# Optimization experiments

Hardware: AMD Instinct MI355X
Metric: run time of the kernel (lower is better)

The kernel has to match this reference:

```python
import jax, jax.numpy as jnp
import numpy as np

S, HID, H, KV, D = 2048, 3584, 16, 8, 256
WINDOW = 1024
SOFTCAP = 50.0
SCALING = 256 ** (-0.5)  # query_pre_attn_scalar ** -0.5
EPS = 1e-6
ROPE_THETA = 10000.0


def _rope_tables(seq_len, dim, theta):
    inv_freq = 1.0 / (theta ** (np.arange(0, dim, 2, dtype=np.float32) / dim))
    t = np.arange(seq_len, dtype=np.float32)
    freqs = np.outer(t, inv_freq)            # [S, D/2]
    emb = np.concatenate([freqs, freqs], -1)  # [S, D]
    return jnp.asarray(np.cos(emb)), jnp.asarray(np.sin(emb))


def setup_inputs() -> dict:
    key = jax.random.key(0)
    ks = jax.random.split(key, 3)
    hidden_states = jax.random.normal(ks[0], (S, HID), jnp.float32)
    w_qkv = jax.random.normal(ks[1], (HID, (H + 2 * KV) * D), jnp.float32) * (HID ** -0.5)
    w_o = jax.random.normal(ks[2], (H * D, HID), jnp.float32) * ((H * D) ** -0.5)
    q_norm_w = jnp.zeros((D,), jnp.float32)  # gemma norm stores weight as (1 + w)
    k_norm_w = jnp.zeros((D,), jnp.float32)
    cos, sin = _rope_tables(S, D, ROPE_THETA)
    return {"hidden_states": hidden_states, "w_qkv": w_qkv, "w_o": w_o,
            "q_norm_w": q_norm_w, "k_norm_w": k_norm_w, "cos": cos, "sin": sin}


def _rms_norm(x, w):
    # gemma-style: fp32 norm, scale by (1 + w); x: [S, h, D]
    xf = x.astype(jnp.float32)
    var = jnp.mean(xf * xf, axis=-1, keepdims=True)
    return (xf * jax.lax.rsqrt(var + EPS) * (1.0 + w)).astype(x.dtype)


def _rotate_half(x):
    x1, x2 = jnp.split(x, 2, axis=-1)
    return jnp.concatenate([-x2, x1], axis=-1)


def _apply_rope(x, cos, sin):
    # x: [S, h, D]; cos/sin: [S, D]
    c = cos[:, None, :]
    s = sin[:, None, :]
    return x * c + _rotate_half(x) * s


def reference(hidden_states, w_qkv, w_o, q_norm_w, k_norm_w, cos, sin):
    qkv = hidden_states @ w_qkv                      # [S, (H+2KV)*D]
    q = qkv[:, : H * D].reshape(S, H, D)
    k = qkv[:, H * D: (H + KV) * D].reshape(S, KV, D)
    v = qkv[:, (H + KV) * D:].reshape(S, KV, D)

    q = _rms_norm(q, q_norm_w)                       # gemma3 q_norm
    k = _rms_norm(k, k_norm_w)                       # gemma3 k_norm
    q = _apply_rope(q, cos, sin)
    k = _apply_rope(k, cos, sin)

    # GQA: expand KV heads to H
    rep = H // KV
    k = jnp.repeat(k, rep, axis=1)                   # [S, H, D]
    v = jnp.repeat(v, rep, axis=1)

    scores = jnp.einsum('shd,thd->hst', q, k) * SCALING  # [H, S, S]
    scores = SOFTCAP * jnp.tanh(scores / SOFTCAP)        # logit softcapping

    i = jnp.arange(S)[:, None]
    j = jnp.arange(S)[None, :]
    allowed = (j <= i) & ((i - j) < WINDOW)              # causal + sliding window
    scores = jnp.where(allowed[None], scores, jnp.float32(-1e30))

    attn = jax.nn.softmax(scores, axis=-1)
    out = jnp.einsum('hst,thd->shd', attn, v).reshape(S, H * D)
    return out @ w_o                                     # [S, HID]
```

## Files before the change

### kernel.cpp

```cpp
#include <hip/hip_runtime.h>
#include <hip/hip_bf16.h>
#include <math.h>

typedef __attribute__((ext_vector_type(8))) short short8;
typedef __attribute__((ext_vector_type(4))) float floatx4;
typedef unsigned short u16;

typedef __attribute__((address_space(1))) const void* gas_ptr;
typedef __attribute__((address_space(3))) void* las_ptr;

__device__ __forceinline__ float bf2f(u16 h) {
  union { unsigned u; float f; } v; v.u = ((unsigned)h) << 16; return v.f;
}
__device__ __forceinline__ u16 f2bf(float f) {
  union { float f; unsigned u; } v; v.f = f;
  unsigned r = v.u + 0x7FFFu + ((v.u >> 16) & 1u);
  return (u16)(r >> 16);
}
__device__ __forceinline__ float ldf_dyn(const void* p, size_t i, bool f32) {
  return f32 ? ((const float*)p)[i] : bf2f(((const u16*)p)[i]);
}
__device__ __forceinline__ short8 load8_dyn(const void* p, size_t idx, bool f32) {
  if (f32) {
    const float* f = (const float*)p;
    float4 a = *(const float4*)(f + idx);
    float4 b = *(const float4*)(f + idx + 4);
    short8 r;
    r[0] = (short)f2bf(a.x); r[1] = (short)f2bf(a.y);
    r[2] = (short)f2bf(a.z); r[3] = (short)f2bf(a.w);
    r[4] = (short)f2bf(b.x); r[5] = (short)f2bf(b.y);
    r[6] = (short)f2bf(b.z); r[7] = (short)f2bf(b.w);
    return r;
  }
  return *(const short8*)((const u16*)p + idx);
}
__device__ __forceinline__ void gl_lds16(const u16* g, u16* l) {
  __builtin_amdgcn_global_load_lds((gas_ptr)g, (las_ptr)l, 16, 0, 0);
}

__global__ void probe_dtype_kernel(const void* hidden, int* flag) {
  __shared__ int cnt;
  if (threadIdx.x == 0) cnt = 0;
  __syncthreads();
  const u16* h = (const u16*)hidden;
  int local = 0;
  for (int i = threadIdx.x; i < 8192; i += 256) {
    u16 u = h[i];
    int e = (u >> 7) & 0xFF;
    if ((e >= 64 && e <= 160) || (u & 0x7FFF) == 0) local++;
  }
  atomicAdd(&cnt, local);
  __syncthreads();
  if (threadIdx.x == 0) *flag = (cnt < 7700) ? 1 : 0;
}

__global__ __launch_bounds__(256) void convert_dyn_kernel(
    const void* __restrict__ src, u16* __restrict__ dst, size_t n,
    const int* __restrict__ flagp)
{
  const bool f32 = (*flagp != 0);
  size_t i = ((size_t)blockIdx.x * 256 + threadIdx.x) * 8;
  if (i < n) *(short8*)(dst + i) = load8_dyn(src, i, f32);
}

__global__ __launch_bounds__(256) void transpose_dyn_kernel(
    const void* __restrict__ src, u16* __restrict__ dst, int R, int C,
    const int* __restrict__ flagp)
{
  const bool f32 = (*flagp != 0);
  const int c0 = blockIdx.x * 64, r0 = blockIdx.y * 64;
  __shared__ __attribute__((aligned(16))) u16 T[64][72];
  const int tid = threadIdx.x;
#pragma unroll
  for (int i = 0; i < 2; i++) {
    int t = tid + i * 256;
    int r = t >> 3, cc = (t & 7) << 3;
    *(short8*)(&T[r][cc]) = load8_dyn(src, (size_t)(r0 + r) * C + c0 + cc, f32);
  }
  __syncthreads();
#pragma unroll
  for (int i = 0; i < 2; i++) {
    int t = tid + i * 256;
    int cr = t >> 3, rc = (t & 7) << 3;
    __attribute__((aligned(16))) u16 tmp[8];
#pragma unroll
    for (int j = 0; j < 8; j++) tmp[j] = T[rc + j][cr];
    *(short8*)(dst + (size_t)(c0 + cr) * R + r0 + rc) = *(const short8*)tmp;
  }
}

#define BAR() __builtin_amdgcn_s_barrier()
#define SCB() __builtin_amdgcn_sched_barrier(0)
#define LGKM0() do { asm volatile("s_waitcnt lgkmcnt(0)" ::: "memory"); SCB(); } while (0)
#define VMW(n) do { asm volatile("s_waitcnt vmcnt(" #n ")" ::: "memory"); SCB(); } while (0)

#define STG_AU(s, u, t) \
  gl_lds16(pa + (size_t)((u) * 64) * K + (size_t)(t) * 64, \
           ldsw + (s) * 32768 + (u) * 4096)
#define STG_BU(s, u, t) \
  gl_lds16(pb + (size_t)((u) * 64) * K + (size_t)(t) * 64, \
           ldsw + (s) * 32768 + 16384 + (u) * 4096)

#define RD_FA(s, miH) do { \
  _Pragma("unroll") \
  for (int m2 = 0; m2 < 4; m2++) { \
    const u16* _r = LDS + (s) * 32768 + wm * 8192 + (miH) * 4096 + m2 * 1024 + lane15 * 64; \
    fa[m2][0] = *(const short8*)(_r + colA0); \
    fa[m2][1] = *(const short8*)(_r + colA1); \
  } \
} while (0)
#define RD_FB(s, niH) do { \
  _Pragma("unroll") \
  for (int n2 = 0; n2 < 2; n2++) { \
    const u16* _r = LDS + (s) * 32768 + 16384 + wn * 4096 + (niH) * 2048 + n2 * 1024 + lane15 * 64; \
    fb[niH][n2][0] = *(const short8*)(_r + colA0); \
    fb[niH][n2][1] = *(const short8*)(_r + colA1); \
  } \
} while (0)
#define MFMA_Q(miH, niH) do { \
  __builtin_amdgcn_s_setprio(1); \
  _Pragma("unroll") \
  for (int m2 = 0; m2 < 4; m2++) \
    _Pragma("unroll") \
    for (int n2 = 0; n2 < 2; n2++) { \
      acc[(miH) * 4 + m2][(niH) * 2 + n2] = __builtin_amdgcn_mfma_f32_16x16x32_bf16( \
          fa[m2][0], fb[niH][n2][0], acc[(miH) * 4 + m2][(niH) * 2 + n2], 0, 0, 0); \
      acc[(miH) * 4 + m2][(niH) * 2 + n2] = __builtin_amdgcn_mfma_f32_16x16x32_bf16( \
          fa[m2][1], fb[niH][n2][1], acc[(miH) * 4 + m2][(niH) * 2 + n2], 0, 0, 0); \
    } \
  __builtin_amdgcn_s_setprio(0); \
  SCB(); \
} while (0)

__global__ __launch_bounds__(512, 2) void gemm8p_kernel(
    const u16* __restrict__ A, const u16* __restrict__ BT, u16* __restrict__ C,
    int M, int N, int K)
{
  __shared__ __attribute__((aligned(16))) u16 LDS[65536];
  const int tid = threadIdx.x;
  const int wave = tid >> 6, lane = tid & 63;
  const int lane15 = lane & 15, quad = lane >> 4;
  const int wm = wave >> 2, wn = wave & 3;
  const int m0 = blockIdx.y * 256, n0 = blockIdx.x * 256;

  const int rloc = wave * 8 + (lane >> 3);
  const int sxor = lane >> 3;
  const int csw = ((lane & 7) ^ sxor) * 8;
  const u16* pa = A + (size_t)(m0 + rloc) * K + csw;
  const u16* pb = BT + (size_t)(n0 + rloc) * K + csw;
  u16* ldsw = LDS + wave * 512;

  const int swz = lane15 & 7;
  const int colA0 = (quad ^ swz) * 8;
  const int colA1 = ((4 + quad) ^ swz) * 8;

  floatx4 acc[8][4];
#pragma unroll
  for (int i = 0; i < 8; i++)
#pragma unroll
    for (int j = 0; j < 4; j++) acc[i][j] = (floatx4){0.f, 0.f, 0.f, 0.f};
  short8 fa[4][2], fb[2][2][2];

  const int NT = K >> 6, NI = NT >> 1;

  STG_AU(0, 0, 0); STG_AU(0, 2, 0);
  STG_BU(0, 0, 0); STG_BU(0, 1, 0);
  STG_BU(0, 2, 0); STG_BU(0, 3, 0);
  STG_AU(0, 1, 0); STG_AU(0, 3, 0);
  STG_AU(1, 0, 1); STG_AU(1, 2, 1);
  STG_BU(1, 0, 1); STG_BU(1, 1, 1);
  STG_BU(1, 2, 1); STG_BU(1, 3, 1);
  VMW(8);
  BAR();

  for (int i = 0; i < NI - 1; i++) {
    const int t1 = 2 * i + 1, t2 = 2 * i + 2, t3 = 2 * i + 3;
    RD_FA(0, 0); RD_FB(0, 0);
    STG_AU(1, 1, t1); STG_AU(1, 3, t1);
    BAR(); LGKM0(); MFMA_Q(0, 0); BAR();
    RD_FB(0, 1);
    STG_AU(0, 0, t2); STG_AU(0, 2, t2);
    BAR(); LGKM0(); MFMA_Q(0, 1); VMW(10); BAR();
    RD_FA(0, 1);
    STG_BU(0, 0, t2); STG_BU(0, 1, t2);
    BAR(); LGKM0(); MFMA_Q(1, 1); BAR();
    STG_BU(0, 2, t2); STG_BU(0, 3, t2);
    BAR(); MFMA_Q(1, 0); VMW(8); BAR();
    RD_FA(1, 0); RD_FB(1, 0);
    STG_AU(0, 1, t2); STG_AU(0, 3, t2);
    BAR(); LGKM0(); MFMA_Q(0, 0); BAR();
    RD_FB(1, 1);
    STG_AU(1, 0, t3); STG_AU(1, 2, t3);
    BAR(); LGKM0(); MFMA_Q(0, 1); VMW(10); BAR();
    RD_FA(1, 1);
    STG_BU(1, 0, t3); STG_BU(1, 1, t3);
    BAR(); LGKM0(); MFMA_Q(1, 1); BAR();
    STG_BU(1, 2, t3); STG_BU(1, 3, t3);
    BAR(); MFMA_Q(1, 0); VMW(8); BAR();
  }

  {
    const int tL = NT - 1;
    RD_FA(0, 0); RD_FB(0, 0);
    STG_AU(1, 1, tL); STG_AU(1, 3, tL);
    BAR(); LGKM0(); MFMA_Q(0, 0); BAR();
    RD_FB(0, 1);
    BAR(); LGKM0(); MFMA_Q(0, 1); VMW(8); BAR();
    RD_FA(0, 1);
    BAR(); LGKM0(); MFMA_Q(1, 1); BAR();
    BAR(); MFMA_Q(1, 0); VMW(2); BAR();
    RD_FA(1, 0); RD_FB(1, 0);
    BAR(); LGKM0(); MFMA_Q(0, 0); BAR();
    RD_FB(1, 1);
    BAR(); LGKM0(); MFMA_Q(0, 1); VMW(0); BAR();
    RD_FA(1, 1);
    BAR(); LGKM0(); MFMA_Q(1, 1); BAR();
    BAR(); MFMA_Q(1, 0);
  }

#pragma unroll
  for (int mi = 0; mi < 8; mi++)
#pragma unroll
    for (int rr = 0; rr < 4; rr++) {
      int m = m0 + wm * 128 + mi * 16 + quad * 4 + rr;
      u16* crow = C + (size_t)m * N + n0 + wn * 64;
#pragma unroll
      for (int ni = 0; ni < 4; ni++) crow[ni * 16 + lane15] = f2bf(acc[mi][ni][rr]);
    }
}

__global__ __launch_bounds__(256) void gemm_bt_kernel(
    const u16* __restrict__ A, const u16* __restrict__ BT, void* __restrict__ C,
    int M, int N, int K, const int* __restrict__ flagp, int cdyn)
{
  __shared__ __attribute__((aligned(16))) u16 As[128 * 32];
  __shared__ __attribute__((aligned(16))) u16 Bs[128 * 32];
  const int tid = threadIdx.x;
  const int wave = tid >> 6, lane = tid & 63;
  const int lane15 = lane & 15, quad = lane >> 4;
  const int wr = (wave >> 1) * 64, wc = (wave & 1) * 64;
  const int m0 = blockIdx.y * 128, n0 = blockIdx.x * 128;

  const int ch0 = wave * 64 + lane;
  const int ch1 = ch0 + 256;
  const int sr0 = ch0 >> 2, sk0 = (ch0 & 3) << 3;
  const int sr1 = ch1 >> 2, sk1 = (ch1 & 3) << 3;
  u16* ldsA0 = &As[wave * 512];
  u16* ldsA1 = &As[2048 + wave * 512];
  u16* ldsB0 = &Bs[wave * 512];
  u16* ldsB1 = &Bs[2048 + wave * 512];
  const u16* pa0 = A + (size_t)(m0 + sr0) * K + sk0;
  const u16* pa1 = A + (size_t)(m0 + sr1) * K + sk1;
  const u16* pb0 = BT + (size_t)(n0 + sr0) * K + sk0;
  const u16* pb1 = BT + (size_t)(n0 + sr1) * K + sk1;

  floatx4 zero = {0.0f, 0.0f, 0.0f, 0.0f};
  floatx4 acc[4][4];
#pragma unroll
  for (int i = 0; i < 4; i++)
#pragma unroll
    for (int j = 0; j < 4; j++) acc[i][j] = zero;

  for (int k0 = 0; k0 < K; k0 += 32) {
    gl_lds16(pa0, ldsA0); gl_lds16(pa1, ldsA1);
    gl_lds16(pb0, ldsB0); gl_lds16(pb1, ldsB1);
    pa0 += 32; pa1 += 32; pb0 += 32; pb1 += 32;
    __syncthreads();
    short8 af[4], bfr[4];
#pragma unroll
    for (int mi = 0; mi < 4; mi++)
      af[mi] = *(const short8*)(&As[(wr + mi * 16 + lane15) * 32 + quad * 8]);
#pragma unroll
    for (int ni = 0; ni < 4; ni++)
      bfr[ni] = *(const short8*)(&Bs[(wc + ni * 16 + lane15) * 32 + quad * 8]);
#pragma unroll
    for (int mi = 0; mi < 4; mi++)
#pragma unroll
      for (int ni = 0; ni < 4; ni++)
        acc[mi][ni] = __builtin_amdgcn_mfma_f32_16x16x32_bf16(
            af[mi], bfr[ni], acc[mi][ni], 0, 0, 0);
    __syncthreads();
  }
  const bool cf32 = cdyn && (*flagp != 0);
  if (cf32) {
    float* Cf = (float*)C;
#pragma unroll
    for (int mi = 0; mi < 4; mi++)
#pragma unroll
      for (int r = 0; r < 4; r++) {
        int m = m0 + wr + mi * 16 + quad * 4 + r;
        float* crow = Cf + (size_t)m * N + n0 + wc;
#pragma unroll
        for (int ni = 0; ni < 4; ni++) crow[ni * 16 + lane15] = acc[mi][ni][r];
      }
  } else {
    u16* Cb = (u16*)C;
#pragma unroll
    for (int mi = 0; mi < 4; mi++)
#pragma unroll
      for (int r = 0; r < 4; r++) {
        int m = m0 + wr + mi * 16 + quad * 4 + r;
        u16* crow = Cb + (size_t)m * N + n0 + wc;
#pragma unroll
        for (int ni = 0; ni < 4; ni++) crow[ni * 16 + lane15] = f2bf(acc[mi][ni][r]);
      }
  }
}

__global__ __launch_bounds__(256) void normrope_kernel(
    u16* __restrict__ qkv, const void* __restrict__ qw,
    const void* __restrict__ kw, const void* __restrict__ cosb,
    const void* __restrict__ sinb, const int* __restrict__ flagp)
{
  const bool f32 = (*flagp != 0);
  const int s = blockIdx.x;
  const int wave = threadIdx.x >> 6, lane = threadIdx.x & 63;
  const int hh = blockIdx.y * 4 + wave;
  const int col = (hh < 16) ? hh * 256 : 4096 + (hh - 16) * 256;
  const void* w = (hh < 16) ? qw : kw;
  u16* row = qkv + (size_t)s * 8192 + col;

  float x[4];
#pragma unroll
  for (int j = 0; j < 4; j++) x[j] = bf2f(row[lane + j * 64]);

  float ss = x[0] * x[0] + x[1] * x[1] + x[2] * x[2] + x[3] * x[3];
#pragma unroll
  for (int off = 32; off > 0; off >>= 1) ss += __shfl_xor(ss, off);
  float inv = rsqrtf(ss * (1.0f / 256.0f) + 1e-6f);

  float y[4];
#pragma unroll
  for (int j = 0; j < 4; j++)
    y[j] = x[j] * inv * (1.0f + ldf_dyn(w, lane + j * 64, f32));
  float rot[4] = {-y[2], -y[3], y[0], y[1]};
#pragma unroll
  for (int j = 0; j < 4; j++) {
    int d = lane + j * 64;
    float c = ldf_dyn(cosb, (size_t)s * 256 + d, f32);
    float sn = ldf_dyn(sinb, (size_t)s * 256 + d, f32);
    row[d] = f2bf(y[j] * c + rot[j] * sn);
  }
}

__global__ __launch_bounds__(256) void vtrans_kernel(
    const u16* __restrict__ qkv, u16* __restrict__ vT)
{
  const int s0 = blockIdx.x * 64, d0 = blockIdx.y * 64, kv = blockIdx.z;
  __shared__ __attribute__((aligned(16))) u16 T[64][72];
  const int tid = threadIdx.x;
#pragma unroll
  for (int i = 0; i < 2; i++) {
    int c = tid + i * 256;
    int r = c >> 3, dc = (c & 7) << 3;
    *(short8*)(&T[r][dc]) =
        *(const short8*)(qkv + (size_t)(s0 + r) * 8192 + 6144 + kv * 256 + d0 + dc);
  }
  __syncthreads();
#pragma unroll
  for (int i = 0; i < 2; i++) {
    int c = tid + i * 256;
    int dr = c >> 3, sc = (c & 7) << 3;
    __attribute__((aligned(16))) u16 tmp[8];
#pragma unroll
    for (int j = 0; j < 8; j++) tmp[j] = T[sc + j][dr];
    *(short8*)(vT + (size_t)kv * 524288 + (size_t)(d0 + dr) * 2048 + s0 + sc) =
        *(const short8*)tmp;
  }
}

__global__ __launch_bounds__(256) void attn_kernel(
    const u16* __restrict__ qkv, const u16* __restrict__ vT,
    u16* __restrict__ aout)
{
  const int h = blockIdx.y, kvh = h >> 1;
  const int q0 = blockIdx.x * 64;
  const int tid = threadIdx.x;
  const int wave = tid >> 6, lane = tid & 63;
  const int lane15 = lane & 15, quad = lane >> 4;

  __shared__ __attribute__((aligned(16))) u16 KVs[256 * 72];
  __shared__ __attribute__((aligned(16))) u16 Ps[4][16 * 72];

  short8 aq[8];
  const u16* qrow = qkv + (size_t)(q0 + wave * 16 + lane15) * 8192 + h * 256;
#pragma unroll
  for (int kt = 0; kt < 8; kt++)
    aq[kt] = *(const short8*)(qrow + kt * 32 + quad * 8);

  floatx4 zero = {0.0f, 0.0f, 0.0f, 0.0f};
  floatx4 accO[16];
#pragma unroll
  for (int i = 0; i < 16; i++) accO[i] = zero;
  float lR[4] = {0.0f, 0.0f, 0.0f, 0.0f};

  const int iRow = q0 + wave * 16 + quad * 4;
  const int kb_lo = (q0 >= 1023) ? ((q0 - 1023) >> 6) : 0;
  const int kb_hi = q0 >> 6;

  for (int kb = kb_lo; kb <= kb_hi; kb++) {
    const int t0 = kb << 6;
#pragma unroll
    for (int i = 0; i < 8; i++) {
      int c = tid + i * 256;
      int r = c >> 5, dc = (c & 31) << 3;
      *(short8*)(&KVs[r * 264 + dc]) =
          *(const short8*)(qkv + (size_t)(t0 + r) * 8192 + 4096 + kvh * 256 + dc);
    }
    __syncthreads();

    const int relHi = q0 + 16 * wave + 15 - t0;
    const int relLo = q0 + 16 * wave - 1023 - t0;
    const int niHiR = relHi >> 4;
    const int niHi = (niHiR > 3) ? 3 : niHiR;
    int niLo = relLo >> 4; if (niLo < 0) niLo = 0;
    const int ktHiR = relHi >> 5;
    const int ktHi = (ktHiR > 1) ? 1 : ktHiR;
    int ktLo = relLo >> 5; if (ktLo < 0) ktLo = 0;

    float pv[4][4];
#pragma unroll
    for (int ni = 0; ni < 4; ni++) {
      if (ni < niLo || ni > niHi) {
        pv[ni][0] = pv[ni][1] = pv[ni][2] = pv[ni][3] = 0.0f;
        continue;
      }
      floatx4 sAcc = zero;
#pragma unroll
      for (int kt = 0; kt < 8; kt++) {
        short8 bk = *(const short8*)(&KVs[(ni * 16 + lane15) * 264 + kt * 32 + quad * 8]);
        sAcc = __builtin_amdgcn_mfma_f32_16x16x32_bf16(aq[kt], bk, sAcc, 0, 0, 0);
      }
#pragma unroll
      for (int r = 0; r < 4; r++) {
        float x = sAcc[r] * 0.00125f;
        float ax = __builtin_fabsf(x);
        float e2 = __expf(ax + ax);
        float t = 1.0f - 2.0f * __builtin_amdgcn_rcpf(e2 + 1.0f);
        float sv = copysignf(t, x) * 50.0f;
        int i_ = iRow + r;
        int j_ = t0 + ni * 16 + lane15;
        bool ok = (j_ <= i_) && (i_ - j_ < 1024);
        pv[ni][r] = ok ? __expf(sv) : 0.0f;
      }
    }
#pragma unroll
    for (int r = 0; r < 4; r++)
      lR[r] += pv[0][r] + pv[1][r] + pv[2][r] + pv[3][r];

#pragma unroll
    for (int ni = 0; ni < 4; ni++)
#pragma unroll
      for (int r = 0; r < 4; r++)
        Ps[wave][(quad * 4 + r) * 72 + ni * 16 + lane15] = f2bf(pv[ni][r]);
    __syncthreads();

#pragma unroll
    for (int i = 0; i < 8; i++) {
      int c = tid + i * 256;
      int dr = c >> 3, tc = (c & 7) << 3;
      *(short8*)(&KVs[dr * 72 + tc]) =
          *(const short8*)(vT + (size_t)kvh * 524288 + (size_t)dr * 2048 + t0 + tc);
    }
    __syncthreads();

#pragma unroll
    for (int ktile = 0; ktile < 2; ktile++) {
      if (ktile < ktLo || ktile > ktHi) continue;
      short8 ap = *(const short8*)(&Ps[wave][lane15 * 72 + ktile * 32 + quad * 8]);
#pragma unroll
      for (int ni = 0; ni < 16; ni++) {
        short8 bv = *(const short8*)(&KVs[(ni * 16 + lane15) * 72 + ktile * 32 + quad * 8]);
        accO[ni] = __builtin_amdgcn_mfma_f32_16x16x32_bf16(ap, bv, accO[ni], 0, 0, 0);
      }
    }
    __syncthreads();
  }

#pragma unroll
  for (int r = 0; r < 4; r++) {
    float l = lR[r];
    l += __shfl_xor(l, 1);
    l += __shfl_xor(l, 2);
    l += __shfl_xor(l, 4);
    l += __shfl_xor(l, 8);
    float invl = 1.0f / l;
    u16* orow = aout + (size_t)(q0 + wave * 16 + quad * 4 + r) * 4096 + h * 256;
#pragma unroll
    for (int ni = 0; ni < 16; ni++)
      orow[ni * 16 + lane15] = f2bf(accO[ni][r] * invl);
  }
}

extern "C" void kernel_launch(void* const* d_in, const int* in_sizes, int n_in,
                              void* d_out, int out_size, void* d_ws, size_t ws_size,
                              hipStream_t stream)
{
  const void* hidden = d_in[0];
  const void* w_qkv  = d_in[1];
  const void* w_o    = d_in[2];
  const void* q_w    = d_in[3];
  const void* k_w    = d_in[4];
  const void* cosb   = d_in[5];
  const void* sinb   = d_in[6];

  char* ws = (char*)d_ws;
  int* flag = (int*)ws;                                   ws += 256;
  u16* qkv  = (u16*)ws;  ws += (size_t)2048 * 8192 * 2;
  u16* vT   = (u16*)ws;  ws += (size_t)8 * 256 * 2048 * 2;
  u16* aout = (u16*)ws;  ws += (size_t)2048 * 4096 * 2;
  u16* hb   = (u16*)ws;  ws += (size_t)2048 * 3584 * 2;
  u16* wT   = (u16*)ws;

  probe_dtype_kernel<<<1, 256, 0, stream>>>(hidden, flag);
  convert_dyn_kernel<<<3584, 256, 0, stream>>>(hidden, hb, (size_t)2048 * 3584, flag);
  transpose_dyn_kernel<<<dim3(128, 56), 256, 0, stream>>>(w_qkv, wT, 3584, 8192, flag);
  gemm8p_kernel<<<dim3(32, 8), 512, 0, stream>>>(hb, wT, qkv, 2048, 8192, 3584);
  normrope_kernel<<<dim3(2048, 6), 256, 0, stream>>>(qkv, q_w, k_w, cosb, sinb, flag);
  transpose_dyn_kernel<<<dim3(56, 64), 256, 0, stream>>>(w_o, wT, 4096, 3584, flag);
  vtrans_kernel<<<dim3(32, 4, 8), 256, 0, stream>>>(qkv, vT);
  attn_kernel<<<dim3(32, 16), 256, 0, stream>>>(qkv, vT, aout);
  gemm_bt_kernel<<<dim3(28, 16), 256, 0, stream>>>(aout, wT, d_out, 2048, 3584, 4096, flag, 1);
}
```

Measured before the change: 583.3 us.

## Replace output-projection GEMM with 8-wave double-buffered swizzled pipelined kernel

Replaces the simple 128x128, 4-wave output projection GEMM (a single LDS buffer with two barriers per 32-wide K step) with a 512-thread, 128x256-tile kernel. The new kernel double-buffers 64-wide K tiles in LDS with an XOR swizzle and interleaves global-to-LDS loads with MFMA quadrants under setprio. The aim is to hide memory latency and cut LDS bank conflicts, mirroring the existing QKV GEMM. The grid shrinks to 224 blocks, which may underfill the CUs, and the larger LDS footprint limits occupancy.

```diff
diff --git a/kernel.cpp b/kernel.cpp
--- a/kernel.cpp
+++ b/kernel.cpp
@@ -229,80 +229,143 @@
     }
 }
 
-__global__ __launch_bounds__(256) void gemm_bt_kernel(
+#define NSTG_A(s, u, t) \
+  gl_lds16(pa + (size_t)((u) * 64) * K + (size_t)(t) * 64, \
+           ldsw + (s) * 24576 + (u) * 4096)
+#define NSTG_B(s, u, t) \
+  gl_lds16(pb + (size_t)((u) * 64) * K + (size_t)(t) * 64, \
+           ldsw + (s) * 24576 + 8192 + (u) * 4096)
+
+#define NRD_FA(s, miH) do { \
+  _Pragma("unroll") \
+  for (int m2 = 0; m2 < 2; m2++) { \
+    const u16* _r = LDS + (s) * 24576 + wm * 4096 + (miH) * 2048 + m2 * 1024 + lane15 * 64; \
+    fa[m2][0] = *(const short8*)(_r + colA0); \
+    fa[m2][1] = *(const short8*)(_r + colA1); \
+  } \
+} while (0)
+#define NRD_FB(s, niH) do { \
+  _Pragma("unroll") \
+  for (int n2 = 0; n2 < 2; n2++) { \
+    const u16* _r = LDS + (s) * 24576 + 8192 + wn * 4096 + (niH) * 2048 + n2 * 1024 + lane15 * 64; \
+    fb[niH][n2][0] = *(const short8*)(_r + colA0); \
+    fb[niH][n2][1] = *(const short8*)(_r + colA1); \
+  } \
+} while (0)
+#define NMFMA_Q(miH, niH) do { \
+  __builtin_amdgcn_s_setprio(1); \
+  _Pragma("unroll") \
+  for (int m2 = 0; m2 < 2; m2++) \
+    _Pragma("unroll") \
+    for (int n2 = 0; n2 < 2; n2++) { \
+      acc[(miH) * 2 + m2][(niH) * 2 + n2] = __builtin_amdgcn_mfma_f32_16x16x32_bf16( \
+          fa[m2][0], fb[niH][n2][0], acc[(miH) * 2 + m2][(niH) * 2 + n2], 0, 0, 0); \
+      acc[(miH) * 2 + m2][(niH) * 2 + n2] = __builtin_amdgcn_mfma_f32_16x16x32_bf16( \
+          fa[m2][1], fb[niH][n2][1], acc[(miH) * 2 + m2][(niH) * 2 + n2], 0, 0, 0); \
+    } \
+  __builtin_amdgcn_s_setprio(0); \
+  SCB(); \
+} while (0)
+
+__global__ __launch_bounds__(512, 2) void gemm8pn_kernel(
     const u16* __restrict__ A, const u16* __restrict__ BT, void* __restrict__ C,
     int M, int N, int K, const int* __restrict__ flagp, int cdyn)
 {
-  __shared__ __attribute__((aligned(16))) u16 As[128 * 32];
-  __shared__ __attribute__((aligned(16))) u16 Bs[128 * 32];
+  __shared__ __attribute__((aligned(16))) u16 LDS[49152];
   const int tid = threadIdx.x;
   const int wave = tid >> 6, lane = tid & 63;
   const int lane15 = lane & 15, quad = lane >> 4;
-  const int wr = (wave >> 1) * 64, wc = (wave & 1) * 64;
-  const int m0 = blockIdx.y * 128, n0 = blockIdx.x * 128;
-
-  const int ch0 = wave * 64 + lane;
-  const int ch1 = ch0 + 256;
-  const int sr0 = ch0 >> 2, sk0 = (ch0 & 3) << 3;
-  const int sr1 = ch1 >> 2, sk1 = (ch1 & 3) << 3;
-  u16* ldsA0 = &As[wave * 512];
-  u16* ldsA1 = &As[2048 + wave * 512];
-  u16* ldsB0 = &Bs[wave * 512];
-  u16* ldsB1 = &Bs[2048 + wave * 512];
-  const u16* pa0 = A + (size_t)(m0 + sr0) * K + sk0;
-  const u16* pa1 = A + (size_t)(m0 + sr1) * K + sk1;
-  const u16* pb0 = BT + (size_t)(n0 + sr0) * K + sk0;
-  const u16* pb1 = BT + (size_t)(n0 + sr1) * K + sk1;
-
-  floatx4 zero = {0.0f, 0.0f, 0.0f, 0.0f};
+  const int wm = wave >> 2, wn = wave & 3;
+  const int m0 = blockIdx.y * 128, n0 = blockIdx.x * 256;
+
+  const int rloc = wave * 8 + (lane >> 3);
+  const int sxor = lane >> 3;
+  const int csw = ((lane & 7) ^ sxor) * 8;
+  const u16* pa = A + (size_t)(m0 + rloc) * K + csw;
+  const u16* pb = BT + (size_t)(n0 + rloc) * K + csw;
+  u16* ldsw = LDS + wave * 512;
+
+  const int swz = lane15 & 7;
+  const int colA0 = (quad ^ swz) * 8;
+  const int colA1 = ((4 + quad) ^ swz) * 8;
+
   floatx4 acc[4][4];
 #pragma unroll
   for (int i = 0; i < 4; i++)
 #pragma unroll
-    for (int j = 0; j < 4; j++) acc[i][j] = zero;
-
-  for (int k0 = 0; k0 < K; k0 += 32) {
-    gl_lds16(pa0, ldsA0); gl_lds16(pa1, ldsA1);
-    gl_lds16(pb0, ldsB0); gl_lds16(pb1, ldsB1);
-    pa0 += 32; pa1 += 32; pb0 += 32; pb1 += 32;
-    __syncthreads();
-    short8 af[4], bfr[4];
-#pragma unroll
-    for (int mi = 0; mi < 4; mi++)
-      af[mi] = *(const short8*)(&As[(wr + mi * 16 + lane15) * 32 + quad * 8]);
-#pragma unroll
-    for (int ni = 0; ni < 4; ni++)
-      bfr[ni] = *(const short8*)(&Bs[(wc + ni * 16 + lane15) * 32 + quad * 8]);
-#pragma unroll
-    for (int mi = 0; mi < 4; mi++)
-#pragma unroll
-      for (int ni = 0; ni < 4; ni++)
-        acc[mi][ni] = __builtin_amdgcn_mfma_f32_16x16x32_bf16(
-            af[mi], bfr[ni], acc[mi][ni], 0, 0, 0);
-    __syncthreads();
-  }
+    for (int j = 0; j < 4; j++) acc[i][j] = (floatx4){0.f, 0.f, 0.f, 0.f};
+  short8 fa[2][2], fb[2][2][2];
+
+  const int NT = K >> 6, NI = NT >> 1;
+
+  NSTG_B(0, 0, 0); NSTG_B(0, 1, 0); NSTG_B(0, 2, 0); NSTG_B(0, 3, 0);
+  NSTG_A(0, 0, 0); NSTG_A(0, 1, 0);
+  NSTG_B(1, 0, 1); NSTG_B(1, 1, 1); NSTG_B(1, 2, 1); NSTG_B(1, 3, 1);
+  NSTG_A(1, 0, 1); NSTG_A(1, 1, 1);
+  VMW(6);
+  BAR();
+
+  for (int i = 0; i < NI - 1; i++) {
+    const int t2 = 2 * i + 2, t3 = 2 * i + 3;
+    NRD_FA(0, 0); NRD_FB(0, 0);
+    BAR(); LGKM0(); NMFMA_Q(0, 0); BAR();
+    NRD_FB(0, 1);
+    BAR(); LGKM0(); NMFMA_Q(0, 1); BAR();
+    NRD_FA(0, 1);
+    NSTG_B(0, 0, t2); NSTG_B(0, 1, t2);
+    BAR(); LGKM0(); NMFMA_Q(1, 1); BAR();
+    NSTG_B(0, 2, t2); NSTG_B(0, 3, t2); NSTG_A(0, 0, t2); NSTG_A(0, 1, t2);
+    BAR(); NMFMA_Q(1, 0); VMW(6); BAR();
+    NRD_FA(1, 0); NRD_FB(1, 0);
+    BAR(); LGKM0(); NMFMA_Q(0, 0); BAR();
+    NRD_FB(1, 1);
+    BAR(); LGKM0(); NMFMA_Q(0, 1); BAR();
+    NRD_FA(1, 1);
+    NSTG_B(1, 0, t3); NSTG_B(1, 1, t3);
+    BAR(); LGKM0(); NMFMA_Q(1, 1); BAR();
+    NSTG_B(1, 2, t3); NSTG_B(1, 3, t3); NSTG_A(1, 0, t3); NSTG_A(1, 1, t3);
+    BAR(); NMFMA_Q(1, 0); VMW(6); BAR();
+  }
+
+  {
+    NRD_FA(0, 0); NRD_FB(0, 0);
+    BAR(); LGKM0(); NMFMA_Q(0, 0); BAR();
+    NRD_FB(0, 1);
+    BAR(); LGKM0(); NMFMA_Q(0, 1); BAR();
+    NRD_FA(0, 1);
+    BAR(); LGKM0(); NMFMA_Q(1, 1); BAR();
+    BAR(); NMFMA_Q(1, 0); VMW(0); BAR();
+    NRD_FA(1, 0); NRD_FB(1, 0);
+    BAR(); LGKM0(); NMFMA_Q(0, 0); BAR();
+    NRD_FB(1, 1);
+    BAR(); LGKM0(); NMFMA_Q(0, 1); BAR();
+    NRD_FA(1, 1);
+    BAR(); LGKM0(); NMFMA_Q(1, 1); BAR();
+    NMFMA_Q(1, 0);
+  }
+
   const bool cf32 = cdyn && (*flagp != 0);
   if (cf32) {
     float* Cf = (float*)C;
 #pragma unroll
     for (int mi = 0; mi < 4; mi++)
 #pragma unroll
-      for (int r = 0; r < 4; r++) {
-        int m = m0 + wr + mi * 16 + quad * 4 + r;
-        float* crow = Cf + (size_t)m * N + n0 + wc;
-#pragma unroll
-        for (int ni = 0; ni < 4; ni++) crow[ni * 16 + lane15] = acc[mi][ni][r];
+      for (int rr = 0; rr < 4; rr++) {
+        int m = m0 + wm * 64 + mi * 16 + quad * 4 + rr;
+        float* crow = Cf + (size_t)m * N + n0 + wn * 64;
+#pragma unroll
+        for (int ni = 0; ni < 4; ni++) crow[ni * 16 + lane15] = acc[mi][ni][rr];
       }
   } else {
     u16* Cb = (u16*)C;
 #pragma unroll
     for (int mi = 0; mi < 4; mi++)
 #pragma unroll
-      for (int r = 0; r < 4; r++) {
-        int m = m0 + wr + mi * 16 + quad * 4 + r;
-        u16* crow = Cb + (size_t)m * N + n0 + wc;
-#pragma unroll
-        for (int ni = 0; ni < 4; ni++) crow[ni * 16 + lane15] = f2bf(acc[mi][ni][r]);
+      for (int rr = 0; rr < 4; rr++) {
+        int m = m0 + wm * 64 + mi * 16 + quad * 4 + rr;
+        u16* crow = Cb + (size_t)m * N + n0 + wn * 64;
+#pragma unroll
+        for (int ni = 0; ni < 4; ni++) crow[ni * 16 + lane15] = f2bf(acc[mi][ni][rr]);
       }
   }
 }
@@ -520,5 +583,5 @@
   transpose_dyn_kernel<<<dim3(56, 64), 256, 0, stream>>>(w_o, wT, 4096, 3584, flag);
   vtrans_kernel<<<dim3(32, 4, 8), 256, 0, stream>>>(qkv, vT);
   attn_kernel<<<dim3(32, 16), 256, 0, stream>>>(qkv, vT, aout);
-  gemm_bt_kernel<<<dim3(28, 16), 256, 0, stream>>>(aout, wT, d_out, 2048, 3584, 4096, flag, 1);
-}
+  gemm8pn_kernel<<<dim3(14, 16), 512, 0, stream>>>(aout, wT, d_out, 2048, 3584, 4096, flag, 1);
+}
```

Result: faster. 539.1 us (-7.6%).
